# Kernel tuning notes

Measured on AMD Instinct MI355X. Metric: run time of the kernel, lower is better.

## Reference

```python
import jax, jax.numpy as jnp
import numpy as np


def setup_inputs() -> dict:
    key = jax.random.key(0)
    ks = jax.random.split(key, 7)
    n, d_in, d_h = 1024, 1024, 512
    scale = 1.0 / np.sqrt(d_in)
    return {
        "vectors": jax.random.normal(ks[0], (n, d_in), dtype=jnp.float32),
        "W_h": jax.random.normal(ks[1], (d_h, d_in), dtype=jnp.float32) * scale,
        "b_h": jax.random.normal(ks[2], (d_h,), dtype=jnp.float32) * 0.01,
        "W_m": jax.random.normal(ks[3], (d_h, d_in), dtype=jnp.float32) * scale,
        "b_m": jax.random.normal(ks[4], (d_h,), dtype=jnp.float32) * 0.01,
        "w2": jax.random.normal(ks[5], (d_h,), dtype=jnp.float32) * (1.0 / np.sqrt(d_h)),
        "b2": jax.random.normal(ks[6], (1,), dtype=jnp.float32) * 0.01,
    }


def reference(vectors, W_h, b_h, W_m, b_m, w2, b2):
    # Two linear projections: [n, d_h]
    h = vectors @ W_h.T + b_h  # head representations
    m = vectors @ W_m.T + b_m  # modifier representations
    # Pairwise broadcast add: pair[i, j, :] = h[i] + m[j]  -> [n, n, d_h]
    pair = jnp.tanh(h[:, None, :] + m[None, :, :])
    # Linear to scalar + squeeze -> [n, n]
    scores = jnp.einsum("ijh,h->ij", pair, w2) + b2[0]
    return scores
```

## Files before the change

kernel.cpp:

```cpp
#include <hip/hip_runtime.h>
#include <hip/hip_bf16.h>

#define D_IN  1024
#define D_H   512
#define L2E2  2.885390081777927f
#define ECLAMP 15.0f

typedef _Float16 half8 __attribute__((ext_vector_type(8)));
typedef _Float16 half4v __attribute__((ext_vector_type(4)));
typedef float f32x4 __attribute__((ext_vector_type(4)));

__global__ __launch_bounds__(256) void cvt_kernel(
    const float* __restrict__ V,
    const float* __restrict__ Wh, const float* __restrict__ Wm,
    _Float16* __restrict__ Vh, _Float16* __restrict__ Wf)
{
  const int idx = blockIdx.x * 256 + threadIdx.x;
  {
    float4 x = ((const float4*)V)[idx];
    half4v o = { (_Float16)x.x, (_Float16)x.y, (_Float16)x.z, (_Float16)x.w };
    ((half4v*)Vh)[idx] = o;
  }
  {
    const float4* p = (idx < 131072) ? ((const float4*)Wh + idx)
                                     : ((const float4*)Wm + (idx - 131072));
    float4 x = *p;
    half4v o = { (_Float16)x.x, (_Float16)x.y, (_Float16)x.z, (_Float16)x.w };
    ((half4v*)Wf)[idx] = o;
  }
}

__global__ __launch_bounds__(256) void proj_mfma_kernel(
    const _Float16* __restrict__ Vh, const _Float16* __restrict__ Wf,
    const float* __restrict__ bh, const float* __restrict__ bm,
    float* __restrict__ C)
{
  const int tid  = threadIdx.x;
  const int lane = tid & 63;
  const int wid  = tid >> 6;
  const int wi   = wid >> 1, wj = wid & 1;
  const int i0   = (blockIdx.x & 15) * 64;
  const int j0   = (blockIdx.x >> 4) * 64;
  const int r16  = lane & 15;
  const int kg   = lane >> 4;

  const _Float16* A0 = Vh + (size_t)(i0 + 32*wi + r16) * 1024 + kg*8;
  const _Float16* A1 = A0 + 16 * 1024;
  const _Float16* B0 = Wf + (size_t)(j0 + 32*wj + r16) * 1024 + kg*8;
  const _Float16* B1 = B0 + 16 * 1024;

  f32x4 acc00 = {0.f,0.f,0.f,0.f}, acc01 = acc00, acc10 = acc00, acc11 = acc00;
  #pragma unroll 4
  for (int k0 = 0; k0 < D_IN; k0 += 32) {
    half8 a0 = *(const half8*)(A0 + k0);
    half8 a1 = *(const half8*)(A1 + k0);
    half8 b0 = *(const half8*)(B0 + k0);
    half8 b1 = *(const half8*)(B1 + k0);
    acc00 = __builtin_amdgcn_mfma_f32_16x16x32_f16(a0, b0, acc00, 0, 0, 0);
    acc01 = __builtin_amdgcn_mfma_f32_16x16x32_f16(a0, b1, acc01, 0, 0, 0);
    acc10 = __builtin_amdgcn_mfma_f32_16x16x32_f16(a1, b0, acc10, 0, 0, 0);
    acc11 = __builtin_amdgcn_mfma_f32_16x16x32_f16(a1, b1, acc11, 0, 0, 0);
  }

  const float* biasp = (j0 < D_H) ? (bh + j0) : (bm + (j0 - D_H));
  #pragma unroll
  for (int fi = 0; fi < 2; ++fi) {
    #pragma unroll
    for (int fj = 0; fj < 2; ++fj) {
      const f32x4 acc = (fi == 0) ? (fj == 0 ? acc00 : acc01)
                                  : (fj == 0 ? acc10 : acc11);
      const int jl = 32*wj + 16*fj + r16;
      const float bias = biasp[jl];
      #pragma unroll
      for (int rr = 0; rr < 4; ++rr) {
        const int il = 32*wi + 16*fi + 4*kg + rr;
        float x = (acc[rr] + bias) * L2E2;
        x = fminf(fmaxf(x, -ECLAMP), ECLAMP);
        C[(size_t)(i0 + il) * 1024 + j0 + jl] = __builtin_amdgcn_exp2f(x);
      }
    }
  }
}

__global__ __launch_bounds__(256) void proj_kernel(
    const float* __restrict__ V,
    const float* __restrict__ Wh, const float* __restrict__ bh,
    const float* __restrict__ Wm, const float* __restrict__ bm,
    float* __restrict__ C)
{
  __shared__ float As[16][68];
  __shared__ float Bs[16][68];

  const int tid = threadIdx.x;
  const int bi  = blockIdx.x & 15;
  const int bj  = blockIdx.x >> 4;
  const int i0  = bi * 64, j0 = bj * 64;
  const int ti  = tid >> 4, tj = tid & 15;
  const int sr  = tid >> 2;
  const int sk  = (tid & 3) << 2;

  const float* Wbase = (j0 < D_H) ? (Wh + (size_t)j0 * D_IN)
                                  : (Wm + (size_t)(j0 - D_H) * D_IN);
  const float* biasp = (j0 < D_H) ? (bh + j0) : (bm + (j0 - D_H));

  const float* arow = V     + (size_t)(i0 + sr) * D_IN + sk;
  const float* brow = Wbase + (size_t)sr        * D_IN + sk;

  float acc[4][4] = {};
  for (int k0 = 0; k0 < D_IN; k0 += 16) {
    float4 av = *(const float4*)(arow + k0);
    float4 bv = *(const float4*)(brow + k0);
    As[sk+0][sr] = av.x; As[sk+1][sr] = av.y; As[sk+2][sr] = av.z; As[sk+3][sr] = av.w;
    Bs[sk+0][sr] = bv.x; Bs[sk+1][sr] = bv.y; Bs[sk+2][sr] = bv.z; Bs[sk+3][sr] = bv.w;
    __syncthreads();
    #pragma unroll
    for (int kk = 0; kk < 16; ++kk) {
      float4 a = *(const float4*)&As[kk][4*ti];
      float4 b = *(const float4*)&Bs[kk][4*tj];
      #pragma unroll
      for (int x = 0; x < 4; ++x)
        #pragma unroll
        for (int y = 0; y < 4; ++y)
          acc[x][y] = fmaf((&a.x)[x], (&b.x)[y], acc[x][y]);
    }
    __syncthreads();
  }

  const int jl = 4 * tj;
  #pragma unroll
  for (int aa = 0; aa < 4; ++aa) {
    const int i = i0 + 4*ti + aa;
    float4 o;
    #pragma unroll
    for (int bb = 0; bb < 4; ++bb) {
      float x = (acc[aa][bb] + biasp[jl+bb]) * L2E2;
      x = fminf(fmaxf(x, -ECLAMP), ECLAMP);
      (&o.x)[bb] = __builtin_amdgcn_exp2f(x);
    }
    *(float4*)(C + (size_t)i * 1024 + j0 + jl) = o;
  }
}

__global__ __launch_bounds__(256) void score_kernel(
    const float* __restrict__ C,
    const float* __restrict__ w2,
    const float* __restrict__ b2,
    float* __restrict__ out)
{
  __shared__ float hs[32][36];
  __shared__ float ms[32][36];
  __shared__ float wred[4];

  const int tid = threadIdx.x;
  const int bi  = blockIdx.x & 31;
  const int bj  = blockIdx.x >> 5;
  const int i0  = bi * 32, j0 = bj * 32;
  const int ti  = tid >> 4, tj = tid & 15;
  const int sr  = tid >> 3;
  const int sk  = (tid & 7) << 2;

  float sw = 0.f;
  for (int t = tid; t < D_H; t += 256) sw += w2[t];
  #pragma unroll
  for (int off = 32; off > 0; off >>= 1) sw += __shfl_down(sw, off, 64);
  if ((tid & 63) == 0) wred[tid >> 6] = sw;

  const float* hrow = C + (size_t)(i0 + sr) * 1024 + sk;
  const float* mrow = C + (size_t)(j0 + sr) * 1024 + D_H + sk;

  float a00 = 0.f, a01 = 0.f, a10 = 0.f, a11 = 0.f;

  for (int k0 = 0; k0 < D_H; k0 += 32) {
    if (k0) __syncthreads();
    float4 hv = *(const float4*)(hrow + k0);
    float4 mv = *(const float4*)(mrow + k0);
    *(float4*)&hs[sr][sk] = hv;
    *(float4*)&ms[sr][sk] = mv;
    __syncthreads();

    #pragma unroll
    for (int g = 0; g < 8; ++g) {
      const int kk = 4 * g;
      const float wA = w2[k0 + kk + 0];
      const float wB = w2[k0 + kk + 1];
      const float wC = w2[k0 + kk + 2];
      const float wD = w2[k0 + kk + 3];
      float4 eh0 = *(const float4*)&hs[2*ti    ][kk];
      float4 eh1 = *(const float4*)&hs[2*ti + 1][kk];
      float4 em0 = *(const float4*)&ms[2*tj    ][kk];
      float4 em1 = *(const float4*)&ms[2*tj + 1][kk];

      #define TERM(EH, EM, ACC)                                        \
      {                                                                \
        float uA = fmaf((EH).x, (EM).x, 1.f);                          \
        float uB = fmaf((EH).y, (EM).y, 1.f);                          \
        float uC = fmaf((EH).z, (EM).z, 1.f);                          \
        float uD = fmaf((EH).w, (EM).w, 1.f);                          \
        float dAB = uA * uB, dCD = uC * uD;                            \
        float nAB = fmaf(wB, uA, wA * uB);                             \
        float nCD = fmaf(wD, uC, wC * uD);                             \
        float den = dAB * dCD;                                         \
        float num = fmaf(nCD, dAB, nAB * dCD);                         \
        ACC = fmaf(num, __builtin_amdgcn_rcpf(den), ACC);              \
      }
      TERM(eh0, em0, a00)
      TERM(eh0, em1, a01)
      TERM(eh1, em0, a10)
      TERM(eh1, em1, a11)
      #undef TERM
    }
  }

  const float base = b2[0] + wred[0] + wred[1] + wred[2] + wred[3];
  const int i = i0 + 2*ti, j = j0 + 2*tj;
  float2 r0, r1;
  r0.x = fmaf(-2.f, a00, base); r0.y = fmaf(-2.f, a01, base);
  r1.x = fmaf(-2.f, a10, base); r1.y = fmaf(-2.f, a11, base);
  *(float2*)(out + (size_t)i       * 1024 + j) = r0;
  *(float2*)(out + (size_t)(i + 1) * 1024 + j) = r1;
}

extern "C" void kernel_launch(void* const* d_in, const int* in_sizes, int n_in,
                              void* d_out, int out_size, void* d_ws, size_t ws_size,
                              hipStream_t stream) {
  const float* V  = (const float*)d_in[0];
  const float* Wh = (const float*)d_in[1];
  const float* bh = (const float*)d_in[2];
  const float* Wm = (const float*)d_in[3];
  const float* bm = (const float*)d_in[4];
  const float* w2 = (const float*)d_in[5];
  const float* b2 = (const float*)d_in[6];
  float* outp = (float*)d_out;

  char* ws = (char*)d_ws;
  float* C = (float*)ws;
  if (ws_size >= (size_t)(8u << 20)) {
    _Float16* Vh = (_Float16*)(ws + (4u << 20));
    _Float16* Wf = (_Float16*)(ws + (6u << 20));
    cvt_kernel<<<dim3(1024), dim3(256), 0, stream>>>(V, Wh, Wm, Vh, Wf);
    proj_mfma_kernel<<<dim3(256), dim3(256), 0, stream>>>(Vh, Wf, bh, bm, C);
  } else {
    proj_kernel<<<dim3(256), dim3(256), 0, stream>>>(V, Wh, bh, Wm, bm, C);
  }
  score_kernel<<<dim3(1024), dim3(256), 0, stream>>>(C, w2, b2, outp);
}
```

Before: 86.23 us.

## Double-buffer score kernel LDS with register prefetch and split projection tiles

The score kernel now prefetches the next k-chunk of h and m into registers while computing the current one, and ping-pongs between two shared-memory buffers. This drops one barrier per iteration and hides global-load latency. The row padding changes from 36 to 34 floats, so stores are split into float2 writes. The float4 reads from odd rows are no longer 16-byte aligned, which may cost LDS bandwidth or rely on unaligned LDS access. The MFMA projection kernel moves to 32x64 tiles with 512 blocks, giving the GPU more blocks to spread over its compute units.

```diff
diff --git a/kernel.cpp b/kernel.cpp
--- a/kernel.cpp
+++ b/kernel.cpp
@@ -39,45 +39,37 @@
   const int lane = tid & 63;
   const int wid  = tid >> 6;
   const int wi   = wid >> 1, wj = wid & 1;
-  const int i0   = (blockIdx.x & 15) * 64;
-  const int j0   = (blockIdx.x >> 4) * 64;
+  const int i0   = (blockIdx.x & 31) * 32;
+  const int j0   = (blockIdx.x >> 5) * 64;
   const int r16  = lane & 15;
   const int kg   = lane >> 4;
 
-  const _Float16* A0 = Vh + (size_t)(i0 + 32*wi + r16) * 1024 + kg*8;
-  const _Float16* A1 = A0 + 16 * 1024;
+  const _Float16* A0 = Vh + (size_t)(i0 + 16*wi + r16) * 1024 + kg*8;
   const _Float16* B0 = Wf + (size_t)(j0 + 32*wj + r16) * 1024 + kg*8;
   const _Float16* B1 = B0 + 16 * 1024;
 
-  f32x4 acc00 = {0.f,0.f,0.f,0.f}, acc01 = acc00, acc10 = acc00, acc11 = acc00;
-  #pragma unroll 4
+  f32x4 acc0 = {0.f,0.f,0.f,0.f}, acc1 = acc0;
+  #pragma unroll 8
   for (int k0 = 0; k0 < D_IN; k0 += 32) {
-    half8 a0 = *(const half8*)(A0 + k0);
-    half8 a1 = *(const half8*)(A1 + k0);
+    half8 a  = *(const half8*)(A0 + k0);
     half8 b0 = *(const half8*)(B0 + k0);
     half8 b1 = *(const half8*)(B1 + k0);
-    acc00 = __builtin_amdgcn_mfma_f32_16x16x32_f16(a0, b0, acc00, 0, 0, 0);
-    acc01 = __builtin_amdgcn_mfma_f32_16x16x32_f16(a0, b1, acc01, 0, 0, 0);
-    acc10 = __builtin_amdgcn_mfma_f32_16x16x32_f16(a1, b0, acc10, 0, 0, 0);
-    acc11 = __builtin_amdgcn_mfma_f32_16x16x32_f16(a1, b1, acc11, 0, 0, 0);
+    acc0 = __builtin_amdgcn_mfma_f32_16x16x32_f16(a, b0, acc0, 0, 0, 0);
+    acc1 = __builtin_amdgcn_mfma_f32_16x16x32_f16(a, b1, acc1, 0, 0, 0);
   }
 
   const float* biasp = (j0 < D_H) ? (bh + j0) : (bm + (j0 - D_H));
   #pragma unroll
-  for (int fi = 0; fi < 2; ++fi) {
-    #pragma unroll
-    for (int fj = 0; fj < 2; ++fj) {
-      const f32x4 acc = (fi == 0) ? (fj == 0 ? acc00 : acc01)
-                                  : (fj == 0 ? acc10 : acc11);
-      const int jl = 32*wj + 16*fj + r16;
-      const float bias = biasp[jl];
-      #pragma unroll
-      for (int rr = 0; rr < 4; ++rr) {
-        const int il = 32*wi + 16*fi + 4*kg + rr;
-        float x = (acc[rr] + bias) * L2E2;
-        x = fminf(fmaxf(x, -ECLAMP), ECLAMP);
-        C[(size_t)(i0 + il) * 1024 + j0 + jl] = __builtin_amdgcn_exp2f(x);
-      }
+  for (int fj = 0; fj < 2; ++fj) {
+    const f32x4 acc = fj ? acc1 : acc0;
+    const int jl = 32*wj + 16*fj + r16;
+    const float bias = biasp[jl];
+    #pragma unroll
+    for (int rr = 0; rr < 4; ++rr) {
+      const int il = 16*wi + 4*kg + rr;
+      float x = (acc[rr] + bias) * L2E2;
+      x = fminf(fmaxf(x, -ECLAMP), ECLAMP);
+      C[(size_t)(i0 + il) * 1024 + j0 + jl] = __builtin_amdgcn_exp2f(x);
     }
   }
 }
@@ -147,8 +139,8 @@
     const float* __restrict__ b2,
     float* __restrict__ out)
 {
-  __shared__ float hs[32][36];
-  __shared__ float ms[32][36];
+  __shared__ float hs[2][32][34];
+  __shared__ float ms[2][32][34];
   __shared__ float wred[4];
 
   const int tid = threadIdx.x;
@@ -168,15 +160,23 @@
   const float* hrow = C + (size_t)(i0 + sr) * 1024 + sk;
   const float* mrow = C + (size_t)(j0 + sr) * 1024 + D_H + sk;
 
+  float4 hv = *(const float4*)(hrow);
+  float4 mv = *(const float4*)(mrow);
+
   float a00 = 0.f, a01 = 0.f, a10 = 0.f, a11 = 0.f;
+  int p = 0;
 
   for (int k0 = 0; k0 < D_H; k0 += 32) {
-    if (k0) __syncthreads();
-    float4 hv = *(const float4*)(hrow + k0);
-    float4 mv = *(const float4*)(mrow + k0);
-    *(float4*)&hs[sr][sk] = hv;
-    *(float4*)&ms[sr][sk] = mv;
+    ((float2*)&hs[p][sr][sk])[0] = make_float2(hv.x, hv.y);
+    ((float2*)&hs[p][sr][sk+2])[0] = make_float2(hv.z, hv.w);
+    ((float2*)&ms[p][sr][sk])[0] = make_float2(mv.x, mv.y);
+    ((float2*)&ms[p][sr][sk+2])[0] = make_float2(mv.z, mv.w);
     __syncthreads();
+
+    if (k0 + 32 < D_H) {
+      hv = *(const float4*)(hrow + k0 + 32);
+      mv = *(const float4*)(mrow + k0 + 32);
+    }
 
     #pragma unroll
     for (int g = 0; g < 8; ++g) {
@@ -185,10 +185,10 @@
       const float wB = w2[k0 + kk + 1];
       const float wC = w2[k0 + kk + 2];
       const float wD = w2[k0 + kk + 3];
-      float4 eh0 = *(const float4*)&hs[2*ti    ][kk];
-      float4 eh1 = *(const float4*)&hs[2*ti + 1][kk];
-      float4 em0 = *(const float4*)&ms[2*tj    ][kk];
-      float4 em1 = *(const float4*)&ms[2*tj + 1][kk];
+      float4 eh0 = *(const float4*)&hs[p][2*ti    ][kk];
+      float4 eh1 = *(const float4*)&hs[p][2*ti + 1][kk];
+      float4 em0 = *(const float4*)&ms[p][2*tj    ][kk];
+      float4 em1 = *(const float4*)&ms[p][2*tj + 1][kk];
 
       #define TERM(EH, EM, ACC)                                        \
       {                                                                \
@@ -209,6 +209,7 @@
       TERM(eh1, em1, a11)
       #undef TERM
     }
+    p ^= 1;
   }
 
   const float base = b2[0] + wred[0] + wred[1] + wred[2] + wred[3];
@@ -238,7 +239,7 @@
     _Float16* Vh = (_Float16*)(ws + (4u << 20));
     _Float16* Wf = (_Float16*)(ws + (6u << 20));
     cvt_kernel<<<dim3(1024), dim3(256), 0, stream>>>(V, Wh, Wm, Vh, Wf);
-    proj_mfma_kernel<<<dim3(256), dim3(256), 0, stream>>>(Vh, Wf, bh, bm, C);
+    proj_mfma_kernel<<<dim3(512), dim3(256), 0, stream>>>(Vh, Wf, bh, bm, C);
   } else {
     proj_kernel<<<dim3(256), dim3(256), 0, stream>>>(V, Wh, bh, Wm, bm, C);
   }
```

New measurement: 87.74 us. About the same (+1.7%).

## Split-K the projection GEMM and double-buffer a larger score tile

Applied to the files above, without the earlier changes.

The projection kernel is now split along K into two halves, giving 512 blocks instead of 256 for better CU coverage. Each half writes exp2 of its partial sum to its own buffer, and the score kernel multiplies the two buffers (exp(a)·exp(b) = exp(a+b)) with a clamp while loading tiles. The score kernel also moves to 64x32 tiles per block with 8 outputs per thread, double-buffered LDS and register prefetch of the next K slice. The trade-off is an extra 4MB intermediate to read and write, plus a different clamping range that can change accuracy.

```diff
diff --git a/kernel.cpp b/kernel.cpp
--- a/kernel.cpp
+++ b/kernel.cpp
@@ -4,7 +4,6 @@
 #define D_IN  1024
 #define D_H   512
 #define L2E2  2.885390081777927f
-#define ECLAMP 15.0f
 
 typedef _Float16 half8 __attribute__((ext_vector_type(8)));
 typedef _Float16 half4v __attribute__((ext_vector_type(4)));
@@ -30,28 +29,33 @@
   }
 }
 
-__global__ __launch_bounds__(256) void proj_mfma_kernel(
+template<int SPLIT>
+__global__ __launch_bounds__(256, 2) void proj_mfma_kernel(
     const _Float16* __restrict__ Vh, const _Float16* __restrict__ Wf,
     const float* __restrict__ bh, const float* __restrict__ bm,
-    float* __restrict__ C)
+    float* __restrict__ P0, float* __restrict__ P1)
 {
   const int tid  = threadIdx.x;
   const int lane = tid & 63;
   const int wid  = tid >> 6;
   const int wi   = wid >> 1, wj = wid & 1;
-  const int i0   = (blockIdx.x & 15) * 64;
-  const int j0   = (blockIdx.x >> 4) * 64;
+  const int tz   = SPLIT ? (blockIdx.x >> 8) : 0;
+  const int tb   = blockIdx.x & 255;
+  const int i0   = (tb & 15) * 64;
+  const int j0   = (tb >> 4) * 64;
   const int r16  = lane & 15;
   const int kg   = lane >> 4;
-
-  const _Float16* A0 = Vh + (size_t)(i0 + 32*wi + r16) * 1024 + kg*8;
+  const int kb   = tz * 512;
+  const int KLEN = SPLIT ? 512 : 1024;
+
+  const _Float16* A0 = Vh + (size_t)(i0 + 32*wi + r16) * 1024 + kb + kg*8;
   const _Float16* A1 = A0 + 16 * 1024;
-  const _Float16* B0 = Wf + (size_t)(j0 + 32*wj + r16) * 1024 + kg*8;
+  const _Float16* B0 = Wf + (size_t)(j0 + 32*wj + r16) * 1024 + kb + kg*8;
   const _Float16* B1 = B0 + 16 * 1024;
 
   f32x4 acc00 = {0.f,0.f,0.f,0.f}, acc01 = acc00, acc10 = acc00, acc11 = acc00;
   #pragma unroll 4
-  for (int k0 = 0; k0 < D_IN; k0 += 32) {
+  for (int k0 = 0; k0 < KLEN; k0 += 32) {
     half8 a0 = *(const half8*)(A0 + k0);
     half8 a1 = *(const half8*)(A1 + k0);
     half8 b0 = *(const half8*)(B0 + k0);
@@ -63,6 +67,8 @@
   }
 
   const float* biasp = (j0 < D_H) ? (bh + j0) : (bm + (j0 - D_H));
+  float* Pz = (SPLIT && tz) ? P1 : P0;
+  const float CL = SPLIT ? 63.f : 15.f;
   #pragma unroll
   for (int fi = 0; fi < 2; ++fi) {
     #pragma unroll
@@ -70,13 +76,13 @@
       const f32x4 acc = (fi == 0) ? (fj == 0 ? acc00 : acc01)
                                   : (fj == 0 ? acc10 : acc11);
       const int jl = 32*wj + 16*fj + r16;
-      const float bias = biasp[jl];
+      const float bias = (tz == 0) ? biasp[jl] : 0.f;
       #pragma unroll
       for (int rr = 0; rr < 4; ++rr) {
         const int il = 32*wi + 16*fi + 4*kg + rr;
         float x = (acc[rr] + bias) * L2E2;
-        x = fminf(fmaxf(x, -ECLAMP), ECLAMP);
-        C[(size_t)(i0 + il) * 1024 + j0 + jl] = __builtin_amdgcn_exp2f(x);
+        x = fminf(fmaxf(x, -CL), CL);
+        Pz[(size_t)(i0 + il) * 1024 + j0 + jl] = __builtin_amdgcn_exp2f(x);
       }
     }
   }
@@ -92,9 +98,7 @@
   __shared__ float Bs[16][68];
 
   const int tid = threadIdx.x;
-  const int bi  = blockIdx.x & 15;
-  const int bj  = blockIdx.x >> 4;
-  const int i0  = bi * 64, j0 = bj * 64;
+  const int i0  = (blockIdx.x & 15) * 64, j0 = (blockIdx.x >> 4) * 64;
   const int ti  = tid >> 4, tj = tid & 15;
   const int sr  = tid >> 2;
   const int sk  = (tid & 3) << 2;
@@ -134,30 +138,33 @@
     #pragma unroll
     for (int bb = 0; bb < 4; ++bb) {
       float x = (acc[aa][bb] + biasp[jl+bb]) * L2E2;
-      x = fminf(fmaxf(x, -ECLAMP), ECLAMP);
+      x = fminf(fmaxf(x, -15.f), 15.f);
       (&o.x)[bb] = __builtin_amdgcn_exp2f(x);
     }
     *(float4*)(C + (size_t)i * 1024 + j0 + jl) = o;
   }
 }
 
-__global__ __launch_bounds__(256) void score_kernel(
-    const float* __restrict__ C,
-    const float* __restrict__ w2,
-    const float* __restrict__ b2,
+template<int SPLIT>
+__global__ __launch_bounds__(256, 2) void score_kernel(
+    const float* __restrict__ P0, const float* __restrict__ P1,
+    const float* __restrict__ w2, const float* __restrict__ b2,
     float* __restrict__ out)
 {
-  __shared__ float hs[32][36];
-  __shared__ float ms[32][36];
+  __shared__ float hs[2][64][34];
+  __shared__ float ms[2][32][34];
   __shared__ float wred[4];
 
   const int tid = threadIdx.x;
-  const int bi  = blockIdx.x & 31;
-  const int bj  = blockIdx.x >> 5;
-  const int i0  = bi * 32, j0 = bj * 32;
+  const int bi  = blockIdx.x & 15;
+  const int bj  = blockIdx.x >> 4;
+  const int i0  = bi * 64, j0 = bj * 32;
   const int ti  = tid >> 4, tj = tid & 15;
-  const int sr  = tid >> 3;
-  const int sk  = (tid & 7) << 2;
+
+  const int sr  = tid >> 2;
+  const int skq = tid & 3;
+  const int smr = tid >> 3;
+  const int smq = tid & 7;
 
   float sw = 0.f;
   for (int t = tid; t < D_H; t += 256) sw += w2[t];
@@ -165,18 +172,54 @@
   for (int off = 32; off > 0; off >>= 1) sw += __shfl_down(sw, off, 64);
   if ((tid & 63) == 0) wred[tid >> 6] = sw;
 
-  const float* hrow = C + (size_t)(i0 + sr) * 1024 + sk;
-  const float* mrow = C + (size_t)(j0 + sr) * 1024 + D_H + sk;
-
-  float a00 = 0.f, a01 = 0.f, a10 = 0.f, a11 = 0.f;
+  const float* hp0 = P0 + (size_t)(i0 + sr) * 1024 + 4*skq;
+  const float* mp0 = P0 + (size_t)(j0 + smr) * 1024 + D_H + 4*smq;
+  const float* hp1 = SPLIT ? (P1 + (size_t)(i0 + sr) * 1024 + 4*skq) : nullptr;
+  const float* mp1 = SPLIT ? (P1 + (size_t)(j0 + smr) * 1024 + D_H + 4*smq) : nullptr;
+
+  float4 ph0 = *(const float4*)(hp0);
+  float4 ph1 = *(const float4*)(hp0 + 16);
+  float4 pm0 = *(const float4*)(mp0);
+  float4 qh0, qh1, qm0;
+  if (SPLIT) {
+    qh0 = *(const float4*)(hp1);
+    qh1 = *(const float4*)(hp1 + 16);
+    qm0 = *(const float4*)(mp1);
+  }
+
+  float acc[4][2] = {};
+  int p = 0;
+
+  #define CLAMP4(D, X, Y)                                              \
+  {                                                                    \
+    (D).x = fminf(fmaxf((X).x * (Y).x, 3.0517578125e-05f), 32768.f);   \
+    (D).y = fminf(fmaxf((X).y * (Y).y, 3.0517578125e-05f), 32768.f);   \
+    (D).z = fminf(fmaxf((X).z * (Y).z, 3.0517578125e-05f), 32768.f);   \
+    (D).w = fminf(fmaxf((X).w * (Y).w, 3.0517578125e-05f), 32768.f);   \
+  }
 
   for (int k0 = 0; k0 < D_H; k0 += 32) {
-    if (k0) __syncthreads();
-    float4 hv = *(const float4*)(hrow + k0);
-    float4 mv = *(const float4*)(mrow + k0);
-    *(float4*)&hs[sr][sk] = hv;
-    *(float4*)&ms[sr][sk] = mv;
+    float4 vh0, vh1, vm0;
+    if (SPLIT) { CLAMP4(vh0, ph0, qh0) CLAMP4(vh1, ph1, qh1) CLAMP4(vm0, pm0, qm0) }
+    else       { vh0 = ph0; vh1 = ph1; vm0 = pm0; }
+    *(float2*)&hs[p][sr][4*skq]      = make_float2(vh0.x, vh0.y);
+    *(float2*)&hs[p][sr][4*skq + 2]  = make_float2(vh0.z, vh0.w);
+    *(float2*)&hs[p][sr][4*skq + 16] = make_float2(vh1.x, vh1.y);
+    *(float2*)&hs[p][sr][4*skq + 18] = make_float2(vh1.z, vh1.w);
+    *(float2*)&ms[p][smr][4*smq]     = make_float2(vm0.x, vm0.y);
+    *(float2*)&ms[p][smr][4*smq + 2] = make_float2(vm0.z, vm0.w);
     __syncthreads();
+
+    if (k0 + 32 < D_H) {
+      ph0 = *(const float4*)(hp0 + k0 + 32);
+      ph1 = *(const float4*)(hp0 + k0 + 48);
+      pm0 = *(const float4*)(mp0 + k0 + 32);
+      if (SPLIT) {
+        qh0 = *(const float4*)(hp1 + k0 + 32);
+        qh1 = *(const float4*)(hp1 + k0 + 48);
+        qm0 = *(const float4*)(mp1 + k0 + 32);
+      }
+    }
 
     #pragma unroll
     for (int g = 0; g < 8; ++g) {
@@ -185,39 +228,47 @@
       const float wB = w2[k0 + kk + 1];
       const float wC = w2[k0 + kk + 2];
       const float wD = w2[k0 + kk + 3];
-      float4 eh0 = *(const float4*)&hs[2*ti    ][kk];
-      float4 eh1 = *(const float4*)&hs[2*ti + 1][kk];
-      float4 em0 = *(const float4*)&ms[2*tj    ][kk];
-      float4 em1 = *(const float4*)&ms[2*tj + 1][kk];
-
-      #define TERM(EH, EM, ACC)                                        \
-      {                                                                \
-        float uA = fmaf((EH).x, (EM).x, 1.f);                          \
-        float uB = fmaf((EH).y, (EM).y, 1.f);                          \
-        float uC = fmaf((EH).z, (EM).z, 1.f);                          \
-        float uD = fmaf((EH).w, (EM).w, 1.f);                          \
-        float dAB = uA * uB, dCD = uC * uD;                            \
-        float nAB = fmaf(wB, uA, wA * uB);                             \
-        float nCD = fmaf(wD, uC, wC * uD);                             \
-        float den = dAB * dCD;                                         \
-        float num = fmaf(nCD, dAB, nAB * dCD);                         \
-        ACC = fmaf(num, __builtin_amdgcn_rcpf(den), ACC);              \
+      float2 em_[2][2], eh_[4][2];
+      #pragma unroll
+      for (int c = 0; c < 2; ++c) {
+        em_[c][0] = *(const float2*)&ms[p][tj + 16*c][kk];
+        em_[c][1] = *(const float2*)&ms[p][tj + 16*c][kk + 2];
       }
-      TERM(eh0, em0, a00)
-      TERM(eh0, em1, a01)
-      TERM(eh1, em0, a10)
-      TERM(eh1, em1, a11)
-      #undef TERM
-    }
-  }
+      #pragma unroll
+      for (int a = 0; a < 4; ++a) {
+        eh_[a][0] = *(const float2*)&hs[p][ti + 16*a][kk];
+        eh_[a][1] = *(const float2*)&hs[p][ti + 16*a][kk + 2];
+      }
+      #pragma unroll
+      for (int a = 0; a < 4; ++a)
+        #pragma unroll
+        for (int c = 0; c < 2; ++c) {
+          float uA = fmaf(eh_[a][0].x, em_[c][0].x, 1.f);
+          float uB = fmaf(eh_[a][0].y, em_[c][0].y, 1.f);
+          float uC = fmaf(eh_[a][1].x, em_[c][1].x, 1.f);
+          float uD = fmaf(eh_[a][1].y, em_[c][1].y, 1.f);
+          float dAB = uA * uB, dCD = uC * uD;
+          float nAB = fmaf(wB, uA, wA * uB);
+          float nCD = fmaf(wD, uC, wC * uD);
+          float den = dAB * dCD;
+          float num = fmaf(nCD, dAB, nAB * dCD);
+          acc[a][c] = fmaf(num, __builtin_amdgcn_rcpf(den), acc[a][c]);
+        }
+    }
+    p ^= 1;
+  }
+  #undef CLAMP4
 
   const float base = b2[0] + wred[0] + wred[1] + wred[2] + wred[3];
-  const int i = i0 + 2*ti, j = j0 + 2*tj;
-  float2 r0, r1;
-  r0.x = fmaf(-2.f, a00, base); r0.y = fmaf(-2.f, a01, base);
-  r1.x = fmaf(-2.f, a10, base); r1.y = fmaf(-2.f, a11, base);
-  *(float2*)(out + (size_t)i       * 1024 + j) = r0;
-  *(float2*)(out + (size_t)(i + 1) * 1024 + j) = r1;
+  #pragma unroll
+  for (int a = 0; a < 4; ++a) {
+    const int i = i0 + ti + 16*a;
+    #pragma unroll
+    for (int c = 0; c < 2; ++c) {
+      const int j = j0 + tj + 16*c;
+      out[(size_t)i * 1024 + j] = fmaf(-2.f, acc[a][c], base);
+    }
+  }
 }
 
 extern "C" void kernel_launch(void* const* d_in, const int* in_sizes, int n_in,
@@ -233,14 +284,23 @@
   float* outp = (float*)d_out;
 
   char* ws = (char*)d_ws;
-  float* C = (float*)ws;
-  if (ws_size >= (size_t)(8u << 20)) {
+  float* P0 = (float*)ws;
+
+  if (ws_size >= (size_t)(12u << 20)) {
+    float*    P1 = (float*)(ws + (4u << 20));
+    _Float16* Vh = (_Float16*)(ws + (8u << 20));
+    _Float16* Wf = (_Float16*)(ws + (10u << 20));
+    cvt_kernel<<<dim3(1024), dim3(256), 0, stream>>>(V, Wh, Wm, Vh, Wf);
+    proj_mfma_kernel<1><<<dim3(512), dim3(256), 0, stream>>>(Vh, Wf, bh, bm, P0, P1);
+    score_kernel<1><<<dim3(512), dim3(256), 0, stream>>>(P0, P1, w2, b2, outp);
+  } else if (ws_size >= (size_t)(8u << 20)) {
     _Float16* Vh = (_Float16*)(ws + (4u << 20));
     _Float16* Wf = (_Float16*)(ws + (6u << 20));
     cvt_kernel<<<dim3(1024), dim3(256), 0, stream>>>(V, Wh, Wm, Vh, Wf);
-    proj_mfma_kernel<<<dim3(256), dim3(256), 0, stream>>>(Vh, Wf, bh, bm, C);
+    proj_mfma_kernel<0><<<dim3(256), dim3(256), 0, stream>>>(Vh, Wf, bh, bm, P0, P0);
+    score_kernel<0><<<dim3(512), dim3(256), 0, stream>>>(P0, P0, w2, b2, outp);
   } else {
-    proj_kernel<<<dim3(256), dim3(256), 0, stream>>>(V, Wh, bh, Wm, bm, C);
-  }
-  score_kernel<<<dim3(1024), dim3(256), 0, stream>>>(C, w2, b2, outp);
-}
+    proj_kernel<<<dim3(256), dim3(256), 0, stream>>>(V, Wh, bh, Wm, bm, P0);
+    score_kernel<0><<<dim3(512), dim3(256), 0, stream>>>(P0, P0, w2, b2, outp);
+  }
+}
```

New measurement: 85.06 us. No clear change (-1.4%).
